# Performance work log

Measured on AMD Instinct MI355X. Metric: run time of the kernel, lower is better.

## Reference

```python
import jax, jax.numpy as jnp
import numpy as np

EMBED = 1024
DMODEL = 1024
NHEAD = 16
HEAD = DMODEL // NHEAD  # 64
EPS = 1e-5


def layer_norm(x, g, b):
    mu = jnp.mean(x, axis=-1, keepdims=True)
    var = jnp.var(x, axis=-1, keepdims=True)
    return (x - mu) / jnp.sqrt(var + EPS) * g + b


def setup_inputs() -> dict:
    key = jax.random.key(0)
    ks = jax.random.split(key, 16)
    s = 0.02
    B, T = 2, 2048
    return {
        "x": jax.random.normal(ks[0], (B, T, EMBED), jnp.float32),
        "wq": jax.random.normal(ks[1], (NHEAD, EMBED, HEAD), jnp.float32) * s,
        "bq": jnp.zeros((NHEAD, HEAD), jnp.float32),
        "wk": jax.random.normal(ks[2], (NHEAD, EMBED, HEAD), jnp.float32) * s,
        "bk": jnp.zeros((NHEAD, HEAD), jnp.float32),
        "wv": jax.random.normal(ks[3], (NHEAD, EMBED, HEAD), jnp.float32) * s,
        "bv": jnp.zeros((NHEAD, HEAD), jnp.float32),
        "ln1_g": jnp.ones((EMBED,), jnp.float32),
        "ln1_b": jnp.zeros((EMBED,), jnp.float32),
        "ln2_g": jnp.ones((DMODEL,), jnp.float32),
        "ln2_b": jnp.zeros((DMODEL,), jnp.float32),
        "w1": jax.random.normal(ks[4], (DMODEL, 4 * DMODEL), jnp.float32) * s,
        "b1": jnp.zeros((4 * DMODEL,), jnp.float32),
        "w2": jax.random.normal(ks[5], (4 * DMODEL, EMBED), jnp.float32) * s,
        "b2": jnp.zeros((EMBED,), jnp.float32),
    }


def reference(x, wq, bq, wk, bk, wv, bv, ln1_g, ln1_b, ln2_g, ln2_b, w1, b1, w2, b2):
    B, T, C = x.shape
    h = layer_norm(x, ln1_g, ln1_b)  # note: residual uses the normalized x (as in source)
    # per-head projections, vectorized over heads: [B,H,T,D]
    q = jnp.einsum('btc,hcd->bhtd', h, wq) + bq[None, :, None, :]
    k = jnp.einsum('btc,hcd->bhtd', h, wk) + bk[None, :, None, :]
    v = jnp.einsum('btc,hcd->bhtd', h, wv) + bv[None, :, None, :]
    scores = jnp.einsum('bhtd,bhsd->bhts', q, k) / jnp.sqrt(jnp.float32(HEAD))
    causal = jnp.tril(jnp.ones((T, T), bool))
    scores = jnp.where(causal[None, None], scores, jnp.finfo(scores.dtype).min)
    wei = jax.nn.softmax(scores, axis=-1)
    attn = jnp.einsum('bhts,bhsd->bhtd', wei, v)
    attn = attn.transpose(0, 2, 1, 3).reshape(B, T, NHEAD * HEAD)  # concat heads
    y = h + attn
    z = layer_norm(y, ln2_g, ln2_b)
    ff = jax.nn.relu(z @ w1 + b1) @ w2 + b2
    return z + ff
```

## Files before the change

kernel.cpp:

```cpp
#include <hip/hip_runtime.h>
#include <hip/hip_bf16.h>
#include <cstdint>
#include <cstddef>

typedef __attribute__((ext_vector_type(8))) short bf16x8;
typedef __attribute__((ext_vector_type(4))) float f32x4;
typedef __attribute__((ext_vector_type(4))) short short4v;
typedef __attribute__((ext_vector_type(2))) unsigned int uint2v;

__device__ inline void gload_lds16(const void* g, void* l) {
  __builtin_amdgcn_global_load_lds((const __attribute__((address_space(1))) void*)g,
                                   (__attribute__((address_space(3))) void*)l, 16, 0, 0);
}

__device__ inline float exp2_fast(float x) {
  float r;
  asm volatile("v_exp_f32 %0, %1" : "=v"(r) : "v"(x));
  return r;
}

__device__ inline unsigned int cvt_pk_bf16(float lo, float hi) {
  unsigned int r;
  asm volatile("v_cvt_pk_bf16_f32 %0, %1, %2" : "=v"(r) : "v"(lo), "v"(hi));
  return r;
}

__global__ void transpose_pack(const float* __restrict__ src, __hip_bfloat16* __restrict__ dst,
                               int R, int C, int ldDst, long zSrcStride, int zDstRow)
{
  __shared__ float tile[64][65];
  src += (size_t)blockIdx.z * zSrcStride;
  const int r0 = blockIdx.y * 64, c0 = blockIdx.x * 64;
  const int t = threadIdx.x;
#pragma unroll
  for (int i = 0; i < 16; ++i) {
    int idx = i * 256 + t;
    int r = idx >> 6, c = idx & 63;
    tile[r][c] = src[(size_t)(r0 + r) * C + c0 + c];
  }
  __syncthreads();
  const int drow0 = blockIdx.z * zDstRow + c0;
#pragma unroll
  for (int i = 0; i < 16; ++i) {
    int idx = i * 256 + t;
    int cc = idx >> 6, rr = idx & 63;
    dst[(size_t)(drow0 + cc) * ldDst + r0 + rr] = __float2bfloat16(tile[rr][cc]);
  }
}

__global__ void ln_fused(const float* __restrict__ x, const float* __restrict__ add,
                         const float* __restrict__ g, const float* __restrict__ bta,
                         float* __restrict__ of32, __hip_bfloat16* __restrict__ obf)
{
  const int row = blockIdx.x;
  const int t = threadIdx.x;
  float4 v = ((const float4*)(x + (size_t)row * 1024))[t];
  if (add) {
    float4 a = ((const float4*)(add + (size_t)row * 1024))[t];
    v.x += a.x; v.y += a.y; v.z += a.z; v.w += a.w;
  }
  float s = v.x + v.y + v.z + v.w;
  float ss = v.x * v.x + v.y * v.y + v.z * v.z + v.w * v.w;
#pragma unroll
  for (int off = 1; off < 64; off <<= 1) {
    s += __shfl_xor(s, off);
    ss += __shfl_xor(ss, off);
  }
  __shared__ float sb[4], ssb[4];
  const int w = t >> 6, lane = t & 63;
  if (lane == 0) { sb[w] = s; ssb[w] = ss; }
  __syncthreads();
  s = sb[0] + sb[1] + sb[2] + sb[3];
  ss = ssb[0] + ssb[1] + ssb[2] + ssb[3];
  const float mu = s * (1.f / 1024.f);
  const float var = ss * (1.f / 1024.f) - mu * mu;
  const float rstd = rsqrtf(var + 1e-5f);
  float4 gv = ((const float4*)g)[t];
  float4 bv = ((const float4*)bta)[t];
  float4 o;
  o.x = (v.x - mu) * rstd * gv.x + bv.x;
  o.y = (v.y - mu) * rstd * gv.y + bv.y;
  o.z = (v.z - mu) * rstd * gv.z + bv.z;
  o.w = (v.w - mu) * rstd * gv.w + bv.w;
  ((float4*)(of32 + (size_t)row * 1024))[t] = o;
  __hip_bfloat16 hb[4] = { __float2bfloat16(o.x), __float2bfloat16(o.y),
                           __float2bfloat16(o.z), __float2bfloat16(o.w) };
  *(short4v*)(obf + (size_t)row * 1024 + t * 4) = *(const short4v*)hb;
}

template<int EPI>
__global__ __launch_bounds__(256, 2) void gemm_bt(
    const __hip_bfloat16* __restrict__ A, const __hip_bfloat16* __restrict__ Bt,
    int N, int K,
    const float* __restrict__ bias,
    const float* __restrict__ bq, const float* __restrict__ bk, const float* __restrict__ bv,
    __hip_bfloat16* __restrict__ oq, __hip_bfloat16* __restrict__ ok, __hip_bfloat16* __restrict__ ovt,
    __hip_bfloat16* __restrict__ obf,
    const float* __restrict__ zres, float* __restrict__ of32)
{
  __shared__ short As[2][128 * 32];
  __shared__ short Bs[2][128 * 32];
  const int t = threadIdx.x;
  const int lane = t & 63;
  const int w = t >> 6;
  const int wm = w >> 1, wn = w & 1;
  const int l15 = lane & 15, lg = lane >> 4;
  const int m0 = blockIdx.y * 128;
  const int n0 = blockIdx.x * 128;

  f32x4 acc[4][4];
#pragma unroll
  for (int i = 0; i < 4; ++i)
#pragma unroll
    for (int j = 0; j < 4; ++j)
#pragma unroll
      for (int e = 0; e < 4; ++e) acc[i][j][e] = 0.f;

  auto STAGE = [&](int buf, int kk0) {
#pragma unroll
    for (int i = 0; i < 2; ++i) {
      int c = t + 256 * i;
      int r = c >> 2, cc = c & 3;
      int kk = (cc ^ ((r >> 1) & 3)) * 8;
      gload_lds16(A + (size_t)(m0 + r) * K + kk0 + kk, (char*)As + buf * 8192 + c * 16);
      gload_lds16(Bt + (size_t)(n0 + r) * K + kk0 + kk, (char*)Bs + buf * 8192 + c * 16);
    }
  };

  STAGE(0, 0);
  int buf = 0;
  for (int k0 = 0; k0 < K; k0 += 32) {
    const int knext = (k0 + 32 < K) ? k0 + 32 : k0;
    STAGE(buf ^ 1, knext);
    asm volatile("s_waitcnt vmcnt(4)" ::: "memory");
    __builtin_amdgcn_s_barrier();
    asm volatile("" ::: "memory");

    bf16x8 af[4], bfr[4];
#pragma unroll
    for (int fm = 0; fm < 4; ++fm) {
      int r = wm * 64 + fm * 16 + l15;
      int kc = lg ^ ((r >> 1) & 3);
      af[fm] = *(const bf16x8*)&As[buf][r * 32 + kc * 8];
    }
#pragma unroll
    for (int fn = 0; fn < 4; ++fn) {
      int r = wn * 64 + fn * 16 + l15;
      int kc = lg ^ ((r >> 1) & 3);
      bfr[fn] = *(const bf16x8*)&Bs[buf][r * 32 + kc * 8];
    }
#pragma unroll
    for (int fm = 0; fm < 4; ++fm)
#pragma unroll
      for (int fn = 0; fn < 4; ++fn)
        acc[fm][fn] = __builtin_amdgcn_mfma_f32_16x16x32_bf16(af[fm], bfr[fn], acc[fm][fn], 0, 0, 0);

    asm volatile("" ::: "memory");
    __builtin_amdgcn_s_barrier();
    buf ^= 1;
  }

#pragma unroll
  for (int fm = 0; fm < 4; ++fm) {
    const int mbase = m0 + wm * 64 + fm * 16 + lg * 4;
#pragma unroll
    for (int fn = 0; fn < 4; ++fn) {
      const int n = n0 + wn * 64 + fn * 16 + l15;
      if (EPI == 0) {
        const int seg = n >> 10;
        const int cn = n & 1023;
        const int h = cn >> 6, d = cn & 63;
        const float* bp = (seg == 0) ? bq : (seg == 1) ? bk : bv;
        const float bias_v = bp[cn];
#pragma unroll
        for (int rg = 0; rg < 4; ++rg) {
          const int m = mbase + rg;
          const int b = m >> 11, tt = m & 2047;
          const size_t bh = (size_t)(b * 16 + h);
          const float val = acc[fm][fn][rg] + bias_v;
          if (seg == 0)      oq[(bh * 2048 + tt) * 64 + d] = __float2bfloat16(val);
          else if (seg == 1) ok[(bh * 2048 + tt) * 64 + d] = __float2bfloat16(val);
          else               ovt[(bh * 64 + d) * 2048 + tt] = __float2bfloat16(val);
        }
      } else if (EPI == 1) {
        const float bias_v = bias[n];
#pragma unroll
        for (int rg = 0; rg < 4; ++rg) {
          const int m = mbase + rg;
          float val = acc[fm][fn][rg] + bias_v;
          val = fmaxf(val, 0.f);
          obf[(size_t)m * N + n] = __float2bfloat16(val);
        }
      } else {
        const float bias_v = bias[n];
#pragma unroll
        for (int rg = 0; rg < 4; ++rg) {
          const int m = mbase + rg;
          const float val = acc[fm][fn][rg] + bias_v;
          of32[(size_t)m * 1024 + n] = zres[(size_t)m * 1024 + n] + val;
        }
      }
    }
  }
}

__global__ __launch_bounds__(256, 3) void flash_attn(
    const __hip_bfloat16* __restrict__ Q, const __hip_bfloat16* __restrict__ Kb,
    const __hip_bfloat16* __restrict__ Vt,
    __hip_bfloat16* __restrict__ Opart, float* __restrict__ Lpart)
{
  __shared__ short Ks[2][64 * 64];
  __shared__ short Vs[2][64 * 64];
  __shared__ short P2[4][32 * 72];
  const int t = threadIdx.x;
  const int lane = t & 63, w = t >> 6;
  const int l15 = lane & 15, lg = lane >> 4;
  const int chunk = blockIdx.x, qblk = blockIdx.y, bh = blockIdx.z;
  const int q0 = qblk * 128;
  const int s_base = chunk * 512;
  if (s_base > q0 + 127) return;
  const int s_hi = (s_base + 512 < q0 + 128) ? s_base + 512 : q0 + 128;
  const int ntiles = (s_hi - s_base) >> 6;
  const int qw = q0 + w * 32;

  const __hip_bfloat16* Qbh = Q + (size_t)bh * 2048 * 64;
  const __hip_bfloat16* Kbh = Kb + (size_t)bh * 2048 * 64;
  const __hip_bfloat16* Vbh = Vt + (size_t)bh * 64 * 2048;

  bf16x8 qf[2][2];
#pragma unroll
  for (int fm = 0; fm < 2; ++fm)
#pragma unroll
    for (int kc = 0; kc < 2; ++kc)
      qf[fm][kc] = *(const bf16x8*)(Qbh + (size_t)(qw + fm * 16 + l15) * 64 + kc * 32 + lg * 8);

  const int srow = (w << 4) + (lane >> 3);
  const int schunk = ((lane & 7) ^ (lane >> 3)) * 8;

  auto STAGE = [&](int bufi, int s0) {
#pragma unroll
    for (int i = 0; i < 2; ++i) {
      const int r = srow + i * 8;
      const int dst = bufi * 8192 + w * 2048 + i * 1024 + lane * 16;
      gload_lds16(Kbh + (size_t)(s0 + r) * 64 + schunk, (char*)Ks + dst);
      gload_lds16(Vbh + (size_t)r * 2048 + s0 + schunk, (char*)Vs + dst);
    }
  };

  f32x4 o_acc[2][4];
  float lpart[2] = {0.f, 0.f};
#pragma unroll
  for (int fm = 0; fm < 2; ++fm)
#pragma unroll
    for (int fd = 0; fd < 4; ++fd)
#pragma unroll
      for (int e = 0; e < 4; ++e) o_acc[fm][fd][e] = 0.f;

  const float C = 0.18033688011112042f;

  STAGE(0, s_base);
  int cur = 0;
  for (int ti = 0; ti < ntiles; ++ti) {
    const int s0 = s_base + ti * 64;
    const int nxt = (ti + 1 < ntiles) ? s0 + 64 : s0;
    STAGE(cur ^ 1, nxt);
    asm volatile("s_waitcnt vmcnt(4)" ::: "memory");
    __builtin_amdgcn_s_barrier();
    asm volatile("" ::: "memory");

    if (s0 <= qw + 31) {
      f32x4 s_acc[2][4];
#pragma unroll
      for (int fm = 0; fm < 2; ++fm)
#pragma unroll
        for (int fn = 0; fn < 4; ++fn)
#pragma unroll
          for (int e = 0; e < 4; ++e) s_acc[fm][fn][e] = 0.f;
#pragma unroll
      for (int kc = 0; kc < 2; ++kc)
#pragma unroll
        for (int fn = 0; fn < 4; ++fn) {
          const int r = fn * 16 + l15;
          bf16x8 kf = *(const bf16x8*)&Ks[cur][r * 64 + ((((kc << 2) | lg) ^ (l15 & 7)) << 3)];
          s_acc[0][fn] = __builtin_amdgcn_mfma_f32_16x16x32_bf16(kf, qf[0][kc], s_acc[0][fn], 0, 0, 0);
          s_acc[1][fn] = __builtin_amdgcn_mfma_f32_16x16x32_bf16(kf, qf[1][kc], s_acc[1][fn], 0, 0, 0);
        }

      const bool needmask = (s0 + 63 > qw);
      float pr[2][4][4];
#pragma unroll
      for (int fm = 0; fm < 2; ++fm) {
        const int qv = qw + fm * 16 + l15;
#pragma unroll
        for (int fn = 0; fn < 4; ++fn)
#pragma unroll
          for (int rg = 0; rg < 4; ++rg) {
            float p = exp2_fast(s_acc[fm][fn][rg] * C);
            if (needmask) {
              const int sg = s0 + fn * 16 + lg * 4 + rg;
              p = (sg <= qv) ? p : 0.f;
            }
            pr[fm][fn][rg] = p;
            lpart[fm] += p;
          }
      }

#pragma unroll
      for (int fm = 0; fm < 2; ++fm)
#pragma unroll
        for (int fn = 0; fn < 4; ++fn) {
          uint2v u;
          u.x = cvt_pk_bf16(pr[fm][fn][0], pr[fm][fn][1]);
          u.y = cvt_pk_bf16(pr[fm][fn][2], pr[fm][fn][3]);
          *(uint2v*)&P2[w][(fm * 16 + l15) * 72 + fn * 16 + lg * 4] = u;
        }

#pragma unroll
      for (int kc = 0; kc < 2; ++kc) {
        bf16x8 pf0 = *(const bf16x8*)&P2[w][(l15) * 72 + kc * 32 + lg * 8];
        bf16x8 pf1 = *(const bf16x8*)&P2[w][(16 + l15) * 72 + kc * 32 + lg * 8];
#pragma unroll
        for (int fd = 0; fd < 4; ++fd) {
          const int r = fd * 16 + l15;
          bf16x8 vf = *(const bf16x8*)&Vs[cur][r * 64 + ((((kc << 2) | lg) ^ (l15 & 7)) << 3)];
          o_acc[0][fd] = __builtin_amdgcn_mfma_f32_16x16x32_bf16(vf, pf0, o_acc[0][fd], 0, 0, 0);
          o_acc[1][fd] = __builtin_amdgcn_mfma_f32_16x16x32_bf16(vf, pf1, o_acc[1][fd], 0, 0, 0);
        }
      }
    }

    asm volatile("" ::: "memory");
    __builtin_amdgcn_s_barrier();
    cur ^= 1;
  }

  const int pslot = ((bh * 16 + qblk) << 2) + chunk;
  __hip_bfloat16* op = Opart + (size_t)pslot * 8192;
#pragma unroll
  for (int fm = 0; fm < 2; ++fm) {
    float l = lpart[fm];
    l += __shfl_xor(l, 16);
    l += __shfl_xor(l, 32);
    const int qloc = w * 32 + fm * 16 + l15;
    if (lg == 0) Lpart[pslot * 128 + qloc] = l;
#pragma unroll
    for (int fd = 0; fd < 4; ++fd) {
      uint2v u;
      u.x = cvt_pk_bf16(o_acc[fm][fd][0], o_acc[fm][fd][1]);
      u.y = cvt_pk_bf16(o_acc[fm][fd][2], o_acc[fm][fd][3]);
      *(uint2v*)(op + (size_t)qloc * 64 + fd * 16 + lg * 4) = u;
    }
  }
}

__global__ void flash_merge(const __hip_bfloat16* __restrict__ Opart,
                            const float* __restrict__ Lpart, float* __restrict__ attn)
{
  const int qblk = blockIdx.x, bh = blockIdx.y;
  const int b = bh >> 4, h = bh & 15;
  const int nch = (qblk >> 2) + 1;
  const int t = threadIdx.x;
  const int r = t >> 1, half = t & 1;
  const int base = (bh * 16 + qblk) << 2;

  float l = 0.f;
  float o[32];
#pragma unroll
  for (int j = 0; j < 32; ++j) o[j] = 0.f;

  for (int ch = 0; ch < nch; ++ch) {
    l += Lpart[(base + ch) * 128 + r];
    const __hip_bfloat16* op = Opart + (size_t)(base + ch) * 8192 + r * 64 + half * 32;
#pragma unroll
    for (int j = 0; j < 4; ++j) {
      bf16x8 v = *(const bf16x8*)(op + j * 8);
#pragma unroll
      for (int e = 0; e < 8; ++e) {
        unsigned int bits = ((unsigned int)(unsigned short)v[e]) << 16;
        o[j * 8 + e] += __uint_as_float(bits);
      }
    }
  }
  const float inv = 1.f / l;
  float* dst = attn + (size_t)(b * 2048 + qblk * 128 + r) * 1024 + h * 64 + half * 32;
#pragma unroll
  for (int j = 0; j < 8; ++j) {
    float4 v4;
    v4.x = o[j * 4 + 0] * inv; v4.y = o[j * 4 + 1] * inv;
    v4.z = o[j * 4 + 2] * inv; v4.w = o[j * 4 + 3] * inv;
    ((float4*)dst)[j] = v4;
  }
}

extern "C" void kernel_launch(void* const* d_in, const int* in_sizes, int n_in,
                              void* d_out, int out_size, void* d_ws, size_t ws_size,
                              hipStream_t stream) {
  const float* x    = (const float*)d_in[0];
  const float* wq   = (const float*)d_in[1];
  const float* bq   = (const float*)d_in[2];
  const float* wk   = (const float*)d_in[3];
  const float* bk   = (const float*)d_in[4];
  const float* wv   = (const float*)d_in[5];
  const float* bv   = (const float*)d_in[6];
  const float* ln1g = (const float*)d_in[7];
  const float* ln1b = (const float*)d_in[8];
  const float* ln2g = (const float*)d_in[9];
  const float* ln2b = (const float*)d_in[10];
  const float* w1   = (const float*)d_in[11];
  const float* b1   = (const float*)d_in[12];
  const float* w2   = (const float*)d_in[13];
  const float* b2   = (const float*)d_in[14];
  float* out = (float*)d_out;

  char* ws = (char*)d_ws;
  const size_t MB = 1024 * 1024;
  __hip_bfloat16* h_bf  = (__hip_bfloat16*)(ws + 0);
  float* Lpart          = (float*)(ws + 0);
  __hip_bfloat16* qb    = (__hip_bfloat16*)(ws + 8 * MB);
  __hip_bfloat16* kb    = (__hip_bfloat16*)(ws + 16 * MB);
  __hip_bfloat16* vtb   = (__hip_bfloat16*)(ws + 24 * MB);
  __hip_bfloat16* ff1   = (__hip_bfloat16*)(ws + 0);
  float* h_f32          = (float*)(ws + 32 * MB);
  float* attn           = (float*)(ws + 48 * MB);
  __hip_bfloat16* Opart = (__hip_bfloat16*)(ws + 64 * MB);
  float* z_f32          = (float*)(ws + 64 * MB);
  __hip_bfloat16* z_bf  = (__hip_bfloat16*)(ws + 80 * MB);
  __hip_bfloat16* wqkvT = (__hip_bfloat16*)(ws + 88 * MB);
  __hip_bfloat16* w1T   = (__hip_bfloat16*)(ws + 96 * MB);
  __hip_bfloat16* w2T   = (__hip_bfloat16*)(ws + 104 * MB);

  transpose_pack<<<dim3(1, 16, 16), 256, 0, stream>>>(wq, wqkvT + 0 * 1024 * 1024, 1024, 64, 1024, 65536, 64);
  transpose_pack<<<dim3(1, 16, 16), 256, 0, stream>>>(wk, wqkvT + 1 * 1024 * 1024, 1024, 64, 1024, 65536, 64);
  transpose_pack<<<dim3(1, 16, 16), 256, 0, stream>>>(wv, wqkvT + 2 * 1024 * 1024, 1024, 64, 1024, 65536, 64);
  transpose_pack<<<dim3(64, 16, 1), 256, 0, stream>>>(w1, w1T, 1024, 4096, 1024, 0, 0);
  transpose_pack<<<dim3(16, 64, 1), 256, 0, stream>>>(w2, w2T, 4096, 1024, 4096, 0, 0);

  ln_fused<<<4096, 256, 0, stream>>>(x, nullptr, ln1g, ln1b, h_f32, h_bf);

  gemm_bt<0><<<dim3(24, 32), 256, 0, stream>>>(h_bf, wqkvT, 3072, 1024,
      nullptr, bq, bk, bv, qb, kb, vtb, nullptr, nullptr, nullptr);

  flash_attn<<<dim3(4, 16, 32), 256, 0, stream>>>(qb, kb, vtb, Opart, Lpart);
  flash_merge<<<dim3(16, 32), 256, 0, stream>>>(Opart, Lpart, attn);

  ln_fused<<<4096, 256, 0, stream>>>(h_f32, attn, ln2g, ln2b, z_f32, z_bf);

  gemm_bt<1><<<dim3(32, 32), 256, 0, stream>>>(z_bf, w1T, 4096, 1024,
      b1, nullptr, nullptr, nullptr, nullptr, nullptr, nullptr, ff1, nullptr, nullptr);

  gemm_bt<2><<<dim3(8, 32), 256, 0, stream>>>(ff1, w2T, 1024, 4096,
      b2, nullptr, nullptr, nullptr, nullptr, nullptr, nullptr, nullptr, z_f32, out);
}
```

Baseline: 267.8 us.

## Widen GEMM tiles to 128x256 with 512 threads and split-K the FFN2 GEMM

Changes the GEMM kernel to use 512-thread blocks with 8 waves and a 128x256 output tile, which raises reuse of the A tile and halves the grid size. The FFN2 GEMM, which previously launched only 256 blocks, is split along K into two partial fp32 outputs. A new merge kernel adds the partials, the bias and the residual. This trades extra fp32 partial traffic and one more launch for better occupancy on the skinny GEMM, and it reuses the workspace regions that held h_f32 and attn for the partials.

```diff
diff --git a/kernel.cpp b/kernel.cpp
--- a/kernel.cpp
+++ b/kernel.cpp
@@ -89,24 +89,25 @@
 }
 
 template<int EPI>
-__global__ __launch_bounds__(256, 2) void gemm_bt(
+__global__ __launch_bounds__(512, 2) void gemm_bt(
     const __hip_bfloat16* __restrict__ A, const __hip_bfloat16* __restrict__ Bt,
-    int N, int K,
+    int N, int Kf, int kLen,
     const float* __restrict__ bias,
     const float* __restrict__ bq, const float* __restrict__ bk, const float* __restrict__ bv,
     __hip_bfloat16* __restrict__ oq, __hip_bfloat16* __restrict__ ok, __hip_bfloat16* __restrict__ ovt,
     __hip_bfloat16* __restrict__ obf,
-    const float* __restrict__ zres, float* __restrict__ of32)
+    float* __restrict__ opart)
 {
   __shared__ short As[2][128 * 32];
-  __shared__ short Bs[2][128 * 32];
+  __shared__ short Bs[2][256 * 32];
   const int t = threadIdx.x;
   const int lane = t & 63;
   const int w = t >> 6;
-  const int wm = w >> 1, wn = w & 1;
+  const int wm = w >> 2, wn = w & 3;
   const int l15 = lane & 15, lg = lane >> 4;
   const int m0 = blockIdx.y * 128;
-  const int n0 = blockIdx.x * 128;
+  const int n0 = blockIdx.x * 256;
+  const int kBase = (EPI == 2) ? (int)blockIdx.z * kLen : 0;
 
   f32x4 acc[4][4];
 #pragma unroll
@@ -117,36 +118,41 @@
       for (int e = 0; e < 4; ++e) acc[i][j][e] = 0.f;
 
   auto STAGE = [&](int buf, int kk0) {
+    {
+      const int r = t >> 2, cc = t & 3;
+      const int kk = (cc ^ ((r >> 1) & 3)) * 8;
+      gload_lds16(A + (size_t)(m0 + r) * Kf + kk0 + kk, (char*)As + buf * 8192 + t * 16);
+    }
 #pragma unroll
     for (int i = 0; i < 2; ++i) {
-      int c = t + 256 * i;
-      int r = c >> 2, cc = c & 3;
-      int kk = (cc ^ ((r >> 1) & 3)) * 8;
-      gload_lds16(A + (size_t)(m0 + r) * K + kk0 + kk, (char*)As + buf * 8192 + c * 16);
-      gload_lds16(Bt + (size_t)(n0 + r) * K + kk0 + kk, (char*)Bs + buf * 8192 + c * 16);
+      const int c = t + 512 * i;
+      const int r = c >> 2, cc = c & 3;
+      const int kk = (cc ^ ((r >> 1) & 3)) * 8;
+      gload_lds16(Bt + (size_t)(n0 + r) * Kf + kk0 + kk, (char*)Bs + buf * 16384 + c * 16);
     }
   };
 
-  STAGE(0, 0);
+  STAGE(0, kBase);
   int buf = 0;
-  for (int k0 = 0; k0 < K; k0 += 32) {
-    const int knext = (k0 + 32 < K) ? k0 + 32 : k0;
+  const int kEnd = kBase + kLen;
+  for (int k0 = kBase; k0 < kEnd; k0 += 32) {
+    const int knext = (k0 + 32 < kEnd) ? k0 + 32 : k0;
     STAGE(buf ^ 1, knext);
-    asm volatile("s_waitcnt vmcnt(4)" ::: "memory");
+    asm volatile("s_waitcnt vmcnt(3)" ::: "memory");
     __builtin_amdgcn_s_barrier();
     asm volatile("" ::: "memory");
 
     bf16x8 af[4], bfr[4];
 #pragma unroll
     for (int fm = 0; fm < 4; ++fm) {
-      int r = wm * 64 + fm * 16 + l15;
-      int kc = lg ^ ((r >> 1) & 3);
+      const int r = wm * 64 + fm * 16 + l15;
+      const int kc = lg ^ ((r >> 1) & 3);
       af[fm] = *(const bf16x8*)&As[buf][r * 32 + kc * 8];
     }
 #pragma unroll
     for (int fn = 0; fn < 4; ++fn) {
-      int r = wn * 64 + fn * 16 + l15;
-      int kc = lg ^ ((r >> 1) & 3);
+      const int r = wn * 64 + fn * 16 + l15;
+      const int kc = lg ^ ((r >> 1) & 3);
       bfr[fn] = *(const bf16x8*)&Bs[buf][r * 32 + kc * 8];
     }
 #pragma unroll
@@ -192,16 +198,32 @@
           obf[(size_t)m * N + n] = __float2bfloat16(val);
         }
       } else {
-        const float bias_v = bias[n];
+        float* op = opart + (size_t)blockIdx.z * 4096 * 1024;
 #pragma unroll
         for (int rg = 0; rg < 4; ++rg) {
           const int m = mbase + rg;
-          const float val = acc[fm][fn][rg] + bias_v;
-          of32[(size_t)m * 1024 + n] = zres[(size_t)m * 1024 + n] + val;
+          op[(size_t)m * 1024 + n] = acc[fm][fn][rg];
         }
       }
     }
   }
+}
+
+__global__ void ffn2_merge(const float* __restrict__ p0, const float* __restrict__ p1,
+                           const float* __restrict__ z, const float* __restrict__ b2,
+                           float* __restrict__ out)
+{
+  const size_t i = ((size_t)blockIdx.x * 256 + threadIdx.x) * 4;
+  const float4 a = *(const float4*)(p0 + i);
+  const float4 b = *(const float4*)(p1 + i);
+  const float4 c = *(const float4*)(z + i);
+  const float4 bb = *(const float4*)(b2 + (i & 1023));
+  float4 o;
+  o.x = c.x + bb.x + a.x + b.x;
+  o.y = c.y + bb.y + a.y + b.y;
+  o.z = c.z + bb.z + a.z + b.z;
+  o.w = c.w + bb.w + a.w + b.w;
+  *(float4*)(out + i) = o;
 }
 
 __global__ __launch_bounds__(256, 3) void flash_attn(
@@ -421,7 +443,9 @@
   __hip_bfloat16* vtb   = (__hip_bfloat16*)(ws + 24 * MB);
   __hip_bfloat16* ff1   = (__hip_bfloat16*)(ws + 0);
   float* h_f32          = (float*)(ws + 32 * MB);
+  float* p0             = (float*)(ws + 32 * MB);
   float* attn           = (float*)(ws + 48 * MB);
+  float* p1             = (float*)(ws + 48 * MB);
   __hip_bfloat16* Opart = (__hip_bfloat16*)(ws + 64 * MB);
   float* z_f32          = (float*)(ws + 64 * MB);
   __hip_bfloat16* z_bf  = (__hip_bfloat16*)(ws + 80 * MB);
@@ -437,17 +461,19 @@
 
   ln_fused<<<4096, 256, 0, stream>>>(x, nullptr, ln1g, ln1b, h_f32, h_bf);
 
-  gemm_bt<0><<<dim3(24, 32), 256, 0, stream>>>(h_bf, wqkvT, 3072, 1024,
-      nullptr, bq, bk, bv, qb, kb, vtb, nullptr, nullptr, nullptr);
+  gemm_bt<0><<<dim3(12, 32), 512, 0, stream>>>(h_bf, wqkvT, 3072, 1024, 1024,
+      nullptr, bq, bk, bv, qb, kb, vtb, nullptr, nullptr);
 
   flash_attn<<<dim3(4, 16, 32), 256, 0, stream>>>(qb, kb, vtb, Opart, Lpart);
   flash_merge<<<dim3(16, 32), 256, 0, stream>>>(Opart, Lpart, attn);
 
   ln_fused<<<4096, 256, 0, stream>>>(h_f32, attn, ln2g, ln2b, z_f32, z_bf);
 
-  gemm_bt<1><<<dim3(32, 32), 256, 0, stream>>>(z_bf, w1T, 4096, 1024,
-      b1, nullptr, nullptr, nullptr, nullptr, nullptr, nullptr, ff1, nullptr, nullptr);
-
-  gemm_bt<2><<<dim3(8, 32), 256, 0, stream>>>(ff1, w2T, 1024, 4096,
-      b2, nullptr, nullptr, nullptr, nullptr, nullptr, nullptr, nullptr, z_f32, out);
-}
+  gemm_bt<1><<<dim3(16, 32), 512, 0, stream>>>(z_bf, w1T, 4096, 1024, 1024,
+      b1, nullptr, nullptr, nullptr, nullptr, nullptr, nullptr, ff1, nullptr);
+
+  gemm_bt<2><<<dim3(4, 32, 2), 512, 0, stream>>>(ff1, w2T, 1024, 4096, 2048,
+      nullptr, nullptr, nullptr, nullptr, nullptr, nullptr, nullptr, nullptr, p0);
+
+  ffn2_merge<<<4096, 256, 0, stream>>>(p0, p1, z_f32, b2, out);
+}
```

New measurement: 263.7 us, median of 2. About the same (-1.5%).
